# Performance work log

Measured on AMD Instinct MI355X. Metric: run time of the kernel, lower is better.

Reference implementation:

```python
import jax, jax.numpy as jnp
import numpy as np

LAMBDA_C = 0.003
CLAMP_MIN = 1e-12
CLAMP_MAX = 1e12


def setup_inputs() -> dict:
    key = jax.random.key(0)
    k1, k2, k3 = jax.random.split(key, 3)
    B, D, C = 4096, 512, 10000
    embeddings = jax.random.normal(k1, (B, D), dtype=jnp.float32)
    labels = jax.random.randint(k2, (B,), 0, C, dtype=jnp.int64)
    centers = jax.random.normal(k3, (C, D), dtype=jnp.float32)  # nn.Parameter(torch.randn(C, D))
    return {"embeddings": embeddings, "labels": labels, "centers": centers}


def reference(embeddings, labels, centers):
    # Original builds a [B, C] distance matrix, masks to the true-label column,
    # clamps every entry to [1e-12, 1e12], sums, and divides by B.
    # Equivalent efficient form: gather centers[labels], per-row squared L2
    # distance (expanded as ||e||^2 + ||c||^2 - 2 e.c, matching the addmm math),
    # plus the constant B*(C-1)*1e-12 contributed by the clamped masked-out zeros.
    B = embeddings.shape[0]
    C = centers.shape[0]
    c_sel = centers[labels]                                  # [B, D]
    dist = (jnp.sum(embeddings * embeddings, axis=1)
            + jnp.sum(c_sel * c_sel, axis=1)
            - 2.0 * jnp.sum(embeddings * c_sel, axis=1))     # [B]
    dist = jnp.clip(dist, CLAMP_MIN, CLAMP_MAX)
    masked_floor = jnp.float32(B * (C - 1)) * jnp.float32(CLAMP_MIN)
    loss = (jnp.sum(dist) + masked_floor) / B
    return LAMBDA_C * loss
```

## Files before the change

### kernel.cpp

```cpp
#include <hip/hip_runtime.h>


#define LAMBDA_C  0.003f
#define CLAMP_MIN 1e-12f
#define CLAMP_MAX 1e12f

static constexpr int B = 4096;
static constexpr int D = 512;
static constexpr int C = 10000;

__global__ __launch_bounds__(256) void row_dist_kernel(
    const float* __restrict__ emb,
    const int*   __restrict__ labels,
    const float* __restrict__ centers,
    float*       __restrict__ row_out)
{
    const int wave = threadIdx.x >> 6;
    const int lane = threadIdx.x & 63;
    const int row  = (blockIdx.x << 2) + wave;

    const int label = labels[row];
    const float4* e4 = (const float4*)(emb     + (size_t)row   * D);
    const float4* c4 = (const float4*)(centers + (size_t)label * D);

    float s = 0.0f;
#pragma unroll
    for (int k = 0; k < 2; ++k) {
        const float4 e = e4[lane + (k << 6)];
        const float4 c = c4[lane + (k << 6)];
        const float dx = e.x - c.x;
        const float dy = e.y - c.y;
        const float dz = e.z - c.z;
        const float dw = e.w - c.w;
        s += dx * dx + dy * dy + dz * dz + dw * dw;
    }

#pragma unroll
    for (int off = 32; off > 0; off >>= 1)
        s += __shfl_down(s, off, 64);

    if (lane == 0) {
        s = fminf(fmaxf(s, CLAMP_MIN), CLAMP_MAX);
        row_out[row] = s;
    }
}

__global__ __launch_bounds__(256) void reduce_kernel(
    const float* __restrict__ row_in,
    float*       __restrict__ out)
{
    const float4* in4 = (const float4*)row_in;
    const int tid = threadIdx.x;

    float s = 0.0f;
#pragma unroll
    for (int i = 0; i < 4; ++i) {
        const float4 v = in4[tid + (i << 8)];
        s += v.x + v.y + v.z + v.w;
    }

#pragma unroll
    for (int off = 32; off > 0; off >>= 1)
        s += __shfl_down(s, off, 64);

    __shared__ float wsum[4];
    if ((tid & 63) == 0) wsum[tid >> 6] = s;
    __syncthreads();

    if (tid == 0) {
        const float total = wsum[0] + wsum[1] + wsum[2] + wsum[3];
        const float masked_floor = (float)B * (float)(C - 1) * CLAMP_MIN;
        out[0] = LAMBDA_C * ((total + masked_floor) / (float)B);
    }
}

extern "C" void kernel_launch(void* const* d_in, const int* in_sizes, int n_in,
                              void* d_out, int out_size, void* d_ws, size_t ws_size,
                              hipStream_t stream)
{
    const float* emb     = (const float*)d_in[0];
    const int*   labels  = (const int*)  d_in[1];
    const float* centers = (const float*)d_in[2];
    float*       out     = (float*)d_out;
    float*       row_buf = (float*)d_ws;

    row_dist_kernel<<<B / 4, 256, 0, stream>>>(emb, labels, centers, row_buf);
    reduce_kernel<<<1, 256, 0, stream>>>(row_buf, out);
}
```

Measured before the change: 73.69 us.

## Fuse row distance and final reduction into one cooperative grid-synced kernel

Merges the per-row distance kernel and the single-block reduction kernel into one cooperative launch. Each wave now handles two rows, each block writes a partial sum, and after a grid-wide sync block 0 reduces the 512 partials. This is meant to remove the second kernel launch and the per-row workspace round trip. In exchange it adds a grid barrier and cooperative-launch overhead, and it halves the number of blocks.

```diff
diff --git a/kernel.cpp b/kernel.cpp
--- a/kernel.cpp
+++ b/kernel.cpp
@@ -1,4 +1,7 @@
 #include <hip/hip_runtime.h>
+#include <hip/hip_cooperative_groups.h>
+
+namespace cg = cooperative_groups;
 
 
 #define LAMBDA_C  0.003f
@@ -9,68 +12,86 @@
 static constexpr int D = 512;
 static constexpr int C = 10000;
 
-__global__ __launch_bounds__(256) void row_dist_kernel(
+static constexpr int THREADS        = 256;
+static constexpr int BLOCKS         = 512;
+static constexpr int WAVES_PER_BLK  = THREADS / 64;
+static constexpr int TOTAL_WAVES    = BLOCKS * WAVES_PER_BLK;
+static constexpr int ROWS_PER_WAVE  = B / TOTAL_WAVES;
+
+__global__ __launch_bounds__(THREADS) void center_loss_fused(
     const float* __restrict__ emb,
     const int*   __restrict__ labels,
     const float* __restrict__ centers,
-    float*       __restrict__ row_out)
+    float*       __restrict__ out,
+    float*       __restrict__ partials)
 {
-    const int wave = threadIdx.x >> 6;
+    const int wid  = threadIdx.x >> 6;
     const int lane = threadIdx.x & 63;
-    const int row  = (blockIdx.x << 2) + wave;
+    const int gw   = (blockIdx.x << 2) | wid;
+    const int row0 = gw * ROWS_PER_WAVE;
 
-    const int label = labels[row];
-    const float4* e4 = (const float4*)(emb     + (size_t)row   * D);
-    const float4* c4 = (const float4*)(centers + (size_t)label * D);
+    const int lab0 = labels[row0];
+    const int lab1 = labels[row0 + 1];
 
-    float s = 0.0f;
+    const float4* e0 = (const float4*)(emb     + (size_t)row0       * D);
+    const float4* e1 = (const float4*)(emb     + (size_t)(row0 + 1) * D);
+    const float4* c0 = (const float4*)(centers + (size_t)lab0       * D);
+    const float4* c1 = (const float4*)(centers + (size_t)lab1       * D);
+
+    float s0 = 0.0f, s1 = 0.0f;
 #pragma unroll
     for (int k = 0; k < 2; ++k) {
-        const float4 e = e4[lane + (k << 6)];
-        const float4 c = c4[lane + (k << 6)];
-        const float dx = e.x - c.x;
-        const float dy = e.y - c.y;
-        const float dz = e.z - c.z;
-        const float dw = e.w - c.w;
-        s += dx * dx + dy * dy + dz * dz + dw * dw;
+        const int idx = lane + (k << 6);
+        const float4 ea = e0[idx];
+        const float4 ca = c0[idx];
+        const float4 eb = e1[idx];
+        const float4 cb = c1[idx];
+        {
+            const float dx = ea.x - ca.x, dy = ea.y - ca.y;
+            const float dz = ea.z - ca.z, dw = ea.w - ca.w;
+            s0 += dx * dx + dy * dy + dz * dz + dw * dw;
+        }
+        {
+            const float dx = eb.x - cb.x, dy = eb.y - cb.y;
+            const float dz = eb.z - cb.z, dw = eb.w - cb.w;
+            s1 += dx * dx + dy * dy + dz * dz + dw * dw;
+        }
     }
 
 #pragma unroll
-    for (int off = 32; off > 0; off >>= 1)
-        s += __shfl_down(s, off, 64);
-
-    if (lane == 0) {
-        s = fminf(fmaxf(s, CLAMP_MIN), CLAMP_MAX);
-        row_out[row] = s;
-    }
-}
-
-__global__ __launch_bounds__(256) void reduce_kernel(
-    const float* __restrict__ row_in,
-    float*       __restrict__ out)
-{
-    const float4* in4 = (const float4*)row_in;
-    const int tid = threadIdx.x;
-
-    float s = 0.0f;
-#pragma unroll
-    for (int i = 0; i < 4; ++i) {
-        const float4 v = in4[tid + (i << 8)];
-        s += v.x + v.y + v.z + v.w;
+    for (int off = 32; off > 0; off >>= 1) {
+        s0 += __shfl_down(s0, off, 64);
+        s1 += __shfl_down(s1, off, 64);
     }
 
-#pragma unroll
-    for (int off = 32; off > 0; off >>= 1)
-        s += __shfl_down(s, off, 64);
-
-    __shared__ float wsum[4];
-    if ((tid & 63) == 0) wsum[tid >> 6] = s;
+    __shared__ float wsum[WAVES_PER_BLK];
+    if (lane == 0) {
+        wsum[wid] = fminf(fmaxf(s0, CLAMP_MIN), CLAMP_MAX)
+                  + fminf(fmaxf(s1, CLAMP_MIN), CLAMP_MAX);
+    }
     __syncthreads();
 
-    if (tid == 0) {
-        const float total = wsum[0] + wsum[1] + wsum[2] + wsum[3];
-        const float masked_floor = (float)B * (float)(C - 1) * CLAMP_MIN;
-        out[0] = LAMBDA_C * ((total + masked_floor) / (float)B);
+    if (threadIdx.x == 0) {
+        partials[blockIdx.x] = wsum[0] + wsum[1] + wsum[2] + wsum[3];
+    }
+
+    cg::this_grid().sync();
+
+    if (blockIdx.x == 0) {
+        float s = partials[threadIdx.x] + partials[threadIdx.x + THREADS];
+#pragma unroll
+        for (int off = 32; off > 0; off >>= 1)
+            s += __shfl_down(s, off, 64);
+
+        __shared__ float w2[WAVES_PER_BLK];
+        if (lane == 0) w2[wid] = s;
+        __syncthreads();
+
+        if (threadIdx.x == 0) {
+            const float total = w2[0] + w2[1] + w2[2] + w2[3];
+            const float masked_floor = (float)B * (float)(C - 1) * CLAMP_MIN;
+            out[0] = LAMBDA_C * ((total + masked_floor) / (float)B);
+        }
     }
 }
 
@@ -78,12 +99,15 @@
                               void* d_out, int out_size, void* d_ws, size_t ws_size,
                               hipStream_t stream)
 {
-    const float* emb     = (const float*)d_in[0];
-    const int*   labels  = (const int*)  d_in[1];
-    const float* centers = (const float*)d_in[2];
-    float*       out     = (float*)d_out;
-    float*       row_buf = (float*)d_ws;
+    const float* emb      = (const float*)d_in[0];
+    const int*   labels   = (const int*)  d_in[1];
+    const float* centers  = (const float*)d_in[2];
+    float*       out      = (float*)d_out;
+    float*       partials = (float*)d_ws;
 
-    row_dist_kernel<<<B / 4, 256, 0, stream>>>(emb, labels, centers, row_buf);
-    reduce_kernel<<<1, 256, 0, stream>>>(row_buf, out);
+    void* args[] = { (void*)&emb, (void*)&labels, (void*)&centers,
+                     (void*)&out, (void*)&partials };
+    hipLaunchCooperativeKernel((void*)center_loss_fused,
+                               dim3(BLOCKS), dim3(THREADS),
+                               args, 0, stream);
 }
```

Result: slower. 124.5 us (+69.0%).
